# Performance work log

Measured on AMD Instinct MI355X. Metric: run time of the kernel, lower is better.

## Reference

```python
import jax, jax.numpy as jnp
import numpy as np
import math

B, S, D, H = 4, 2048, 1024, 16
DK = D // H  # 64
THETA = 10000.0


def setup_inputs() -> dict:
    key = jax.random.key(0)
    ks = jax.random.split(key, 5)
    std = 0.02
    return {
        "x": jax.random.normal(ks[0], (B, S, D), dtype=jnp.float32),
        "Wq": jax.random.normal(ks[1], (D, D), dtype=jnp.float32) * std,
        "Wk": jax.random.normal(ks[2], (D, D), dtype=jnp.float32) * std,
        "Wv": jax.random.normal(ks[3], (D, D), dtype=jnp.float32) * std,
        "Wo": jax.random.normal(ks[4], (D, D), dtype=jnp.float32) * std / math.sqrt(2 * 12),
        "token_positions": jnp.arange(S, dtype=jnp.int32),
    }


def _rope(x, pos):
    # x: [B, H, S, DK]; pos: [S]. Interleaved-pair rotary embedding.
    inv_freq = THETA ** (-jnp.arange(0, DK, 2, dtype=jnp.float32) / DK)  # [DK/2]
    ang = pos.astype(jnp.float32)[:, None] * inv_freq[None, :]  # [S, DK/2]
    cos, sin = jnp.cos(ang), jnp.sin(ang)
    x1, x2 = x[..., 0::2], x[..., 1::2]  # [B, H, S, DK/2]
    r1 = x1 * cos - x2 * sin
    r2 = x1 * sin + x2 * cos
    return jnp.stack([r1, r2], axis=-1).reshape(x.shape)


def reference(x, Wq, Wk, Wv, Wo, token_positions):
    b, s, d = x.shape
    Q = x @ Wq
    K = x @ Wk
    V = x @ Wv
    # [B, S, D] -> [B, H, S, DK]
    def split(t):
        return t.reshape(b, s, H, DK).transpose(0, 2, 1, 3)
    Qh, Kh, Vh = split(Q), split(K), split(V)
    Qh = _rope(Qh, token_positions)
    Kh = _rope(Kh, token_positions)
    scores = jnp.einsum('bhqd,bhkd->bhqk', Qh, Kh) / math.sqrt(DK)
    causal = jnp.tril(jnp.ones((s, s), dtype=bool))
    scores = jnp.where(causal, scores, -jnp.inf)
    probs = jax.nn.softmax(scores, axis=-1)
    out = jnp.einsum('bhqk,bhkd->bhqd', probs, Vh)
    out = out.transpose(0, 2, 1, 3).reshape(b, s, d)
    return out @ Wo
```

## Files before the change

kernel.cpp:

```cpp
#include <hip/hip_runtime.h>
#include <hip/hip_bf16.h>

#define B_N 4
#define S_LEN 2048
#define D_MODEL 1024
#define N_HEAD 16
#define D_HEAD 64
#define M_ROWS (B_N * S_LEN)

typedef short bf16x8 __attribute__((ext_vector_type(8)));
typedef short bf16x4 __attribute__((ext_vector_type(4)));
typedef float f32x4 __attribute__((ext_vector_type(4)));

#if __has_builtin(__builtin_amdgcn_mfma_f32_16x16x16bf16_1k)
#define HAVE_MFMA16 1
#else
#define HAVE_MFMA16 0
#endif

__device__ __forceinline__ unsigned short f2bf(float f) {
  union { float f; unsigned int u; } v; v.f = f;
  unsigned int r = v.u + 0x7FFFu + ((v.u >> 16) & 1u);
  return (unsigned short)(r >> 16);
}
__device__ __forceinline__ float bf2f(unsigned short u) {
  union { unsigned int u; float f; } v; v.u = ((unsigned int)u) << 16;
  return v.f;
}
__device__ __forceinline__ unsigned int pkbf(float a, float b) {
  union { __hip_bfloat162 h; unsigned int u; } cv;
  cv.h = __float22bfloat162_rn(make_float2(a, b));
  return cv.u;
}
__device__ __forceinline__ bf16x8 ld8(const unsigned short* p) {
  return *reinterpret_cast<const bf16x8*>(p);
}
__device__ __forceinline__ bf16x4 ld4(const unsigned short* p) {
  return *reinterpret_cast<const bf16x4*>(p);
}
__device__ __forceinline__ void glds16(const unsigned short* g, unsigned short* l) {
  __builtin_amdgcn_global_load_lds(
      (const __attribute__((address_space(1))) unsigned int*)g,
      (__attribute__((address_space(3))) unsigned int*)l, 16, 0, 0);
}

__global__ __launch_bounds__(256) void rope_tab_k(const int* __restrict__ pos,
                                                  float2* __restrict__ tab) {
  const int idx = blockIdx.x * 256 + threadIdx.x;
  const int s = idx >> 5;
  const int i = idx & 31;
  const float inv = exp2f(-(float)i * 0.41524101186092029f);
  const float ang = (float)pos[s] * inv;
  tab[idx] = make_float2(cosf(ang), sinf(ang));
}

__global__ __launch_bounds__(256) void cast_k(const float* __restrict__ X,
                                              unsigned short* __restrict__ Y) {
  const size_t i = ((size_t)blockIdx.x * 256 + threadIdx.x) * 8;
  const float4 a = *reinterpret_cast<const float4*>(X + i);
  const float4 b = *reinterpret_cast<const float4*>(X + i + 4);
  union { unsigned int u[4]; uint4 v; } o;
  o.u[0] = pkbf(a.x, a.y); o.u[1] = pkbf(a.z, a.w);
  o.u[2] = pkbf(b.x, b.y); o.u[3] = pkbf(b.z, b.w);
  *reinterpret_cast<uint4*>(Y + i) = o.v;
}

__global__ __launch_bounds__(256) void wtrans_k(
    const float* __restrict__ W0, const float* __restrict__ W1,
    const float* __restrict__ W2, const float* __restrict__ W3,
    unsigned short* __restrict__ T0, unsigned short* __restrict__ T1,
    unsigned short* __restrict__ T2, unsigned short* __restrict__ T3) {
  const int z = blockIdx.z;
  const float* __restrict__ W = (z == 0) ? W0 : (z == 1) ? W1 : (z == 2) ? W2 : W3;
  unsigned short* __restrict__ T = (z == 0) ? T0 : (z == 1) ? T1 : (z == 2) ? T2 : T3;
  __shared__ __align__(16) unsigned short tile[64][72];
  const int kb = blockIdx.x * 64;
  const int nb = blockIdx.y * 64;
#pragma unroll
  for (int it = 0; it < 2; ++it) {
    const int chunk = it * 256 + threadIdx.x;
    const int r = chunk >> 3;
    const int c8 = (chunk & 7) * 8;
    const float* src = W + (size_t)(kb + r) * D_MODEL + nb + c8;
    const float4 a = *reinterpret_cast<const float4*>(src);
    const float4 b = *reinterpret_cast<const float4*>(src + 4);
    union { unsigned int u[4]; uint4 v; } o;
    o.u[0] = pkbf(a.x, a.y); o.u[1] = pkbf(a.z, a.w);
    o.u[2] = pkbf(b.x, b.y); o.u[3] = pkbf(b.z, b.w);
    *reinterpret_cast<uint4*>(&tile[r][c8]) = o.v;
  }
  __syncthreads();
#pragma unroll
  for (int it = 0; it < 2; ++it) {
    const int chunk = it * 256 + threadIdx.x;
    const int n = chunk >> 3;
    const int k8 = (chunk & 7) * 8;
    __align__(16) unsigned short vals[8];
#pragma unroll
    for (int j = 0; j < 8; ++j) vals[j] = tile[k8 + j][n];
    *reinterpret_cast<uint4*>(T + (size_t)(nb + n) * D_MODEL + kb + k8) =
        *reinterpret_cast<const uint4*>(vals);
  }
}

__global__ __launch_bounds__(256) void gemm2_k(
    const unsigned short* __restrict__ A, const unsigned short* __restrict__ W,
    unsigned short* __restrict__ Qo, unsigned short* __restrict__ Ko,
    unsigned short* __restrict__ VTo, float* __restrict__ OF,
    const float2* __restrict__ tab, const int mode) {
  __shared__ __align__(16) unsigned short smem[4][64][68];
  unsigned short* As = &smem[0][0][0];
  unsigned short* Bs = As + 128 * 32;

  const int tid = threadIdx.x;
  const int lane = tid & 63;
  const int w = tid >> 6;
  const int l15 = lane & 15;
  const int l4 = lane >> 4;

  const int row0 = blockIdx.x * 128;
  const int col0 = blockIdx.y * 128;

  const int srow = w * 32 + (lane >> 2);
  const int scol = (lane & 3) * 8;
  const unsigned short* ga = A + (size_t)(row0 + srow) * D_MODEL + scol;
  const unsigned short* gb = W + (size_t)(col0 + srow) * D_MODEL + scol;
  unsigned short* la = &As[(w * 32) * 32];
  unsigned short* lb = &Bs[(w * 32) * 32];

  const int wrow = (w & 1) * 64;
  const int wcol = (w >> 1) * 64;

  f32x4 acc[4][4];
  const f32x4 fz = {0.f, 0.f, 0.f, 0.f};
#pragma unroll
  for (int m = 0; m < 4; ++m)
#pragma unroll
    for (int n = 0; n < 4; ++n) acc[m][n] = fz;

  for (int kb = 0; kb < D_MODEL; kb += 32) {
    glds16(ga + kb, la);
    glds16(ga + 16 * D_MODEL + kb, la + 16 * 32);
    glds16(gb + kb, lb);
    glds16(gb + 16 * D_MODEL + kb, lb + 16 * 32);
    __syncthreads();
    bf16x8 af[4], bfr[4];
#pragma unroll
    for (int m = 0; m < 4; ++m) af[m] = ld8(&As[(wrow + m * 16 + l15) * 32 + l4 * 8]);
#pragma unroll
    for (int n = 0; n < 4; ++n) bfr[n] = ld8(&Bs[(wcol + n * 16 + l15) * 32 + l4 * 8]);
#pragma unroll
    for (int m = 0; m < 4; ++m)
#pragma unroll
      for (int n = 0; n < 4; ++n)
        acc[m][n] = __builtin_amdgcn_mfma_f32_16x16x32_bf16(af[m], bfr[n], acc[m][n], 0, 0, 0);
    __syncthreads();
  }

  if (mode == 1) {
#pragma unroll
    for (int n = 0; n < 4; ++n) {
      const int gcol = col0 + wcol + n * 16 + l15;
#pragma unroll
      for (int m = 0; m < 4; ++m)
#pragma unroll
        for (int r = 0; r < 4; ++r)
          OF[(size_t)(row0 + wrow + m * 16 + l4 * 4 + r) * D_MODEL + gcol] = acc[m][n][r];
    }
    return;
  }
}

__global__ __launch_bounds__(512, 2) void gemm8_k(
    const unsigned short* __restrict__ A, const unsigned short* __restrict__ W,
    unsigned short* __restrict__ Qo, unsigned short* __restrict__ Ko,
    unsigned short* __restrict__ VTo, const float2* __restrict__ tab) {
  __shared__ __align__(16) unsigned short smem[2][2][256 * 64];

  const int tid = threadIdx.x;
  const int lane = tid & 63;
  const int w = tid >> 6;
  const int l15 = lane & 15;
  const int l4 = lane >> 4;
  const int wm = w >> 2;
  const int wn = w & 3;

  const int row0 = blockIdx.x * 256;
  const int col0 = blockIdx.y * 256;

  const int srow = lane >> 3;
  const int schunk = (lane & 7) ^ ((lane >> 4) & 2);
  const unsigned short* gA = A + (size_t)(row0 + w * 8 + srow) * D_MODEL + schunk * 8;
  const unsigned short* gB = W + (size_t)(col0 + w * 8 + srow) * D_MODEL + schunk * 8;

  const int kx = (l15 & 4) ? 16 : 0;
  const int kc0 = (l4 * 8) ^ kx;
  const int kc1 = (32 + l4 * 8) ^ kx;

  f32x4 acc[8][4];
  const f32x4 fz = {0.f, 0.f, 0.f, 0.f};
#pragma unroll
  for (int m = 0; m < 8; ++m)
#pragma unroll
    for (int n = 0; n < 4; ++n) acc[m][n] = fz;

#define G8_STAGE(SL, T)                                                        \
  do {                                                                         \
    asm volatile("" ::: "memory");                                             \
    const size_t ko_ = (size_t)(T) * 64;                                       \
    unsigned short* sa_ = &smem[SL][0][w * 512];                               \
    unsigned short* sb_ = &smem[SL][1][w * 512];                               \
    _Pragma("unroll") for (int j = 0; j < 4; ++j) {                            \
      glds16(gA + ko_ + (size_t)j * 64 * D_MODEL, sa_ + j * 4096);             \
      glds16(gB + ko_ + (size_t)j * 64 * D_MODEL, sb_ + j * 4096);             \
    }                                                                          \
    asm volatile("" ::: "memory");                                             \
  } while (0)

#define G8_PHASE(SL, MH, NH)                                                   \
  do {                                                                         \
    const unsigned short* As_ = &smem[SL][0][0];                               \
    const unsigned short* Bs_ = &smem[SL][1][0];                               \
    bf16x8 af_[4][2], bf_[2][2];                                               \
    _Pragma("unroll") for (int mi = 0; mi < 4; ++mi) {                         \
      const int rr_ = (wm * 128 + ((MH) * 4 + mi) * 16 + l15) * 64;            \
      af_[mi][0] = ld8(As_ + rr_ + kc0);                                       \
      af_[mi][1] = ld8(As_ + rr_ + kc1);                                       \
    }                                                                          \
    _Pragma("unroll") for (int ni = 0; ni < 2; ++ni) {                         \
      const int cc_ = (wn * 64 + ((NH) * 2 + ni) * 16 + l15) * 64;             \
      bf_[ni][0] = ld8(Bs_ + cc_ + kc0);                                       \
      bf_[ni][1] = ld8(Bs_ + cc_ + kc1);                                       \
    }                                                                          \
    __builtin_amdgcn_s_barrier();                                              \
    __builtin_amdgcn_s_setprio(1);                                             \
    _Pragma("unroll") for (int mi = 0; mi < 4; ++mi)                           \
      _Pragma("unroll") for (int ni = 0; ni < 2; ++ni) {                       \
        acc[(MH) * 4 + mi][(NH) * 2 + ni] =                                    \
            __builtin_amdgcn_mfma_f32_16x16x32_bf16(                           \
                af_[mi][0], bf_[ni][0], acc[(MH) * 4 + mi][(NH) * 2 + ni],     \
                0, 0, 0);                                                      \
        acc[(MH) * 4 + mi][(NH) * 2 + ni] =                                    \
            __builtin_amdgcn_mfma_f32_16x16x32_bf16(                           \
                af_[mi][1], bf_[ni][1], acc[(MH) * 4 + mi][(NH) * 2 + ni],     \
                0, 0, 0);                                                      \
      }                                                                        \
    __builtin_amdgcn_s_setprio(0);                                             \
    __builtin_amdgcn_s_barrier();                                              \
  } while (0)

  G8_STAGE(0, 0);
  G8_STAGE(1, 1);

  for (int i = 0; i < 8; ++i) {
    asm volatile("s_waitcnt vmcnt(8)" ::: "memory");
    __builtin_amdgcn_s_barrier();
    G8_PHASE(0, 0, 0);
    G8_PHASE(0, 0, 1);
    G8_PHASE(0, 1, 0);
    G8_PHASE(0, 1, 1);
    if (i < 7) {
      G8_STAGE(0, 2 * i + 2);
      asm volatile("s_waitcnt vmcnt(8)" ::: "memory");
    } else {
      asm volatile("s_waitcnt vmcnt(0)" ::: "memory");
    }
    __builtin_amdgcn_s_barrier();
    G8_PHASE(1, 0, 0);
    G8_PHASE(1, 0, 1);
    G8_PHASE(1, 1, 0);
    G8_PHASE(1, 1, 1);
    if (i < 7) G8_STAGE(1, 2 * i + 3);
  }
  asm volatile("" ::: "memory");

  unsigned short(*T)[68] =
      (unsigned short(*)[68])(&smem[0][0][0] + w * 4352);
  const int gcb = col0 + wn * 64;
  const bool isV = (gcb >= 2048);
  const int lr = lane >> 3;
  const int lc = lane & 7;

#pragma unroll
  for (int p = 0; p < 2; ++p) {
    if (!isV) {
#pragma unroll
      for (int mi = 0; mi < 4; ++mi)
#pragma unroll
        for (int n = 0; n < 4; ++n)
#pragma unroll
          for (int r = 0; r < 4; ++r)
            T[mi * 16 + l4 * 4 + r][n * 16 + l15] = f2bf(acc[p * 4 + mi][n][r]);
    } else {
#pragma unroll
      for (int mi = 0; mi < 4; ++mi)
#pragma unroll
        for (int n = 0; n < 4; ++n)
#pragma unroll
          for (int r = 0; r < 4; ++r)
            T[n * 16 + l15][mi * 16 + l4 * 4 + r] = f2bf(acc[p * 4 + mi][n][r]);
    }
    if (!isV) {
      const bool isQ = (gcb < 1024);
      unsigned short* O = isQ ? Qo : Ko;
      const float qs = isQ ? 0.18033688011112042f : 1.0f;
      const int cbase = gcb & 1023;
#pragma unroll
      for (int rg = 0; rg < 8; ++rg) {
        const int trow = rg * 8 + lr;
        const int grow = row0 + wm * 128 + p * 64 + trow;
        const int s = grow & (S_LEN - 1);
        const bf16x8 vv = ld8(&T[trow][lc * 8]);
        const float4 tA = *reinterpret_cast<const float4*>(&tab[s * 32 + lc * 4]);
        const float4 tB = *reinterpret_cast<const float4*>(&tab[s * 32 + lc * 4 + 2]);
        float x[8];
#pragma unroll
        for (int j = 0; j < 8; ++j) x[j] = bf2f((unsigned short)vv[j]);
        union { unsigned int u[4]; uint4 v; } o;
        o.u[0] = pkbf((x[0] * tA.x - x[1] * tA.y) * qs, (x[0] * tA.y + x[1] * tA.x) * qs);
        o.u[1] = pkbf((x[2] * tA.z - x[3] * tA.w) * qs, (x[2] * tA.w + x[3] * tA.z) * qs);
        o.u[2] = pkbf((x[4] * tB.x - x[5] * tB.y) * qs, (x[4] * tB.y + x[5] * tB.x) * qs);
        o.u[3] = pkbf((x[6] * tB.z - x[7] * tB.w) * qs, (x[6] * tB.w + x[7] * tB.z) * qs);
        *reinterpret_cast<uint4*>(O + (size_t)grow * D_MODEL + cbase + lc * 8) = o.v;
      }
    } else {
      const int vc0 = gcb - 2048;
      const int h = vc0 >> 6;
      const int bb = row0 >> 11;
      const int s0 = (row0 & (S_LEN - 1)) + wm * 128 + p * 64;
#pragma unroll
      for (int rg = 0; rg < 8; ++rg) {
        const int dk = rg * 8 + lr;
        const bf16x8 vv = ld8(&T[dk][lc * 8]);
        *reinterpret_cast<bf16x8*>(
            VTo + ((size_t)((bb << 4) + h) * 64 + dk) * S_LEN + s0 + lc * 8) = vv;
      }
    }
  }
#undef G8_STAGE
#undef G8_PHASE
}

__global__ __launch_bounds__(512) void attn6_k(
    const unsigned short* __restrict__ Q, const unsigned short* __restrict__ K,
    const unsigned short* __restrict__ VT, unsigned short* __restrict__ O) {
  const int pair = blockIdx.x;
  const int h = blockIdx.y;
  const int b = blockIdx.z;
  const int tid = threadIdx.x;
  const int w = tid >> 6;
  const int lane = tid & 63;
  const int l15 = lane & 15;
  const int l4 = lane >> 4;

  __shared__ __align__(16) unsigned short Ks[64][72];
  __shared__ __align__(16) unsigned short Vs[64][72];
#if !HAVE_MFMA16
  __shared__ __align__(16) unsigned short Ps[8][16][72];
#endif

  const f32x4 fz = {0.f, 0.f, 0.f, 0.f};
  const unsigned short* kbase = K + (size_t)b * S_LEN * D_MODEL + h * D_HEAD;
  const unsigned short* vbase = VT + (size_t)((b << 4) + h) * 64 * S_LEN;

  const int rr = tid >> 3;
  const int c8 = (tid & 7) * 8;

  for (int half = 0; half < 2; ++half) {
    const int qt = half ? (15 - pair) : pair;
    const int qb = qt * 128;
    const int qw0 = qb + w * 16;

    bf16x8 qf[2];
#pragma unroll
    for (int kc = 0; kc < 2; ++kc)
      qf[kc] = ld8(Q + (size_t)(b * S_LEN + qw0 + l15) * D_MODEL +
                   h * D_HEAD + kc * 32 + l4 * 8);

    f32x4 o[4];
#pragma unroll
    for (int d = 0; d < 4; ++d) o[d] = fz;
    float lsum = 0.f;

    const int nkt = qb / 64 + 2;
    uint4 kreg = *reinterpret_cast<const uint4*>(kbase + (size_t)rr * D_MODEL + c8);
    uint4 vreg = *reinterpret_cast<const uint4*>(vbase + (size_t)rr * S_LEN + c8);

    for (int kt = 0; kt < nkt; ++kt) {
      const int kb0 = kt * 64;
      *reinterpret_cast<uint4*>(&Ks[rr][c8]) = kreg;
      *reinterpret_cast<uint4*>(&Vs[rr][c8]) = vreg;
      if (kt + 1 < nkt) {
        const int nb0 = kb0 + 64;
        kreg = *reinterpret_cast<const uint4*>(kbase + (size_t)(nb0 + rr) * D_MODEL + c8);
        vreg = *reinterpret_cast<const uint4*>(vbase + (size_t)rr * S_LEN + nb0 + c8);
      }
      __syncthreads();

      if (kb0 <= qw0 + 15) {
        f32x4 s[4];
#pragma unroll
        for (int n = 0; n < 4; ++n) {
          const bf16x8 kf0 = ld8(&Ks[n * 16 + l15][l4 * 8]);
          const bf16x8 kf1 = ld8(&Ks[n * 16 + l15][32 + l4 * 8]);
          f32x4 a0 = __builtin_amdgcn_mfma_f32_16x16x32_bf16(kf0, qf[0], fz, 0, 0, 0);
          s[n] = __builtin_amdgcn_mfma_f32_16x16x32_bf16(kf1, qf[1], a0, 0, 0, 0);
        }
        bf16x4 pf[4];
        const bool full = (kb0 + 63 <= qw0);
        const int q = qw0 + l15;
        float su = lsum;
#pragma unroll
        for (int n = 0; n < 4; ++n) {
          float e[4];
          if (full) {
#pragma unroll
            for (int r = 0; r < 4; ++r) e[r] = exp2f(s[n][r]);
          } else {
#pragma unroll
            for (int r = 0; r < 4; ++r) {
              const int key = kb0 + n * 16 + l4 * 4 + r;
              const float v = exp2f(s[n][r]);
              e[r] = (key <= q) ? v : 0.f;
            }
          }
          su += (e[0] + e[1]) + (e[2] + e[3]);
          union { unsigned int u[2]; bf16x4 v; } pk;
          pk.u[0] = pkbf(e[0], e[1]);
          pk.u[1] = pkbf(e[2], e[3]);
          pf[n] = pk.v;
        }
        lsum = su;

#if HAVE_MFMA16
#pragma unroll
        for (int d = 0; d < 4; ++d) {
          bf16x4 vfc[4];
#pragma unroll
          for (int c = 0; c < 4; ++c) vfc[c] = ld4(&Vs[d * 16 + l15][c * 16 + l4 * 4]);
#pragma unroll
          for (int c = 0; c < 4; ++c)
            o[d] = __builtin_amdgcn_mfma_f32_16x16x16bf16_1k(vfc[c], pf[c], o[d], 0, 0, 0);
        }
#else
#pragma unroll
        for (int n = 0; n < 4; ++n)
          *reinterpret_cast<bf16x4*>(&Ps[w][l15][n * 16 + l4 * 4]) = pf[n];
        bf16x8 pfr[2];
#pragma unroll
        for (int kc = 0; kc < 2; ++kc)
          pfr[kc] = ld8(&Ps[w][l15][kc * 32 + l4 * 8]);
#pragma unroll
        for (int d = 0; d < 4; ++d) {
          const bf16x8 vf0 = ld8(&Vs[d * 16 + l15][l4 * 8]);
          const bf16x8 vf1 = ld8(&Vs[d * 16 + l15][32 + l4 * 8]);
          o[d] = __builtin_amdgcn_mfma_f32_16x16x32_bf16(vf0, pfr[0], o[d], 0, 0, 0);
          o[d] = __builtin_amdgcn_mfma_f32_16x16x32_bf16(vf1, pfr[1], o[d], 0, 0, 0);
        }
#endif
      }
      __syncthreads();
    }

    float s = lsum;
    s += __shfl_xor(s, 16);
    s += __shfl_xor(s, 32);
    const float li = 1.0f / s;
    unsigned short* op = O + (size_t)(b * S_LEN + qw0 + l15) * D_MODEL +
                         h * D_HEAD + l4 * 4;
#pragma unroll
    for (int d = 0; d < 4; ++d) {
      union { unsigned int u[2]; uint2 v; } ov;
      ov.u[0] = pkbf(o[d][0] * li, o[d][1] * li);
      ov.u[1] = pkbf(o[d][2] * li, o[d][3] * li);
      *reinterpret_cast<uint2*>(op + d * 16) = ov.v;
    }
  }
}

extern "C" void kernel_launch(void* const* d_in, const int* in_sizes, int n_in,
                              void* d_out, int out_size, void* d_ws, size_t ws_size,
                              hipStream_t stream) {
  const float* x  = (const float*)d_in[0];
  const float* Wq = (const float*)d_in[1];
  const float* Wk = (const float*)d_in[2];
  const float* Wv = (const float*)d_in[3];
  const float* Wo = (const float*)d_in[4];
  const int* pos  = (const int*)d_in[5];
  float* out = (float*)d_out;

  char* ws = (char*)d_ws;
  const size_t big = (size_t)M_ROWS * D_MODEL * 2;
  const size_t wsz = (size_t)D_MODEL * D_MODEL * 2;
  unsigned short* xb  = (unsigned short*)(ws + 0 * big);
  unsigned short* Qb  = (unsigned short*)(ws + 1 * big);
  unsigned short* Kb  = (unsigned short*)(ws + 2 * big);
  unsigned short* VT  = (unsigned short*)(ws + 3 * big);
  unsigned short* Wqkvt = (unsigned short*)(ws + 4 * big);
  unsigned short* Wot   = (unsigned short*)(ws + 4 * big + 3 * wsz);
  float2* tab = (float2*)d_out;

  rope_tab_k<<<dim3(S_LEN * 32 / 256), 256, 0, stream>>>(pos, tab);
  cast_k<<<dim3(M_ROWS * D_MODEL / 2048), 256, 0, stream>>>(x, xb);
  wtrans_k<<<dim3(16, 16, 4), 256, 0, stream>>>(
      Wq, Wk, Wv, Wo, Wqkvt, Wqkvt + (size_t)D_MODEL * D_MODEL,
      Wqkvt + 2 * (size_t)D_MODEL * D_MODEL, Wot);
  gemm8_k<<<dim3(M_ROWS / 256, 3 * D_MODEL / 256), 512, 0, stream>>>(
      xb, Wqkvt, Qb, Kb, VT, tab);
  attn6_k<<<dim3(8, N_HEAD, B_N), 512, 0, stream>>>(Qb, Kb, VT, Qb);
  gemm2_k<<<dim3(M_ROWS / 128, D_MODEL / 128), 256, 0, stream>>>(
      Qb, Wot, nullptr, nullptr, nullptr, out, nullptr, 1);
}
```

Baseline: 295.6 us.

## Interleave QKV GEMM global-to-LDS loads with MFMA phases at finer granularity

Rewrites the QKV projection GEMM pipeline. Each K-step's A/B tiles are split into half-tiles (128 rows), and one half-tile load is issued inside each compute phase, so loads are spread across all eight phases instead of issued in bulk between phase groups. The LDS swizzle is changed to an XOR over 8 chunks, and launch bounds drop to one block per CU. Also simplifies gemm2_k by removing unused mode parameters. The finer waitcnt scheduling is meant to hide global latency better, at the risk of more barriers and possible lower occupancy.

After: 456.0 us. 1.54x slower.

```diff
diff --git a/kernel.cpp b/kernel.cpp
--- a/kernel.cpp
+++ b/kernel.cpp
@@ -105,9 +105,7 @@
 
 __global__ __launch_bounds__(256) void gemm2_k(
     const unsigned short* __restrict__ A, const unsigned short* __restrict__ W,
-    unsigned short* __restrict__ Qo, unsigned short* __restrict__ Ko,
-    unsigned short* __restrict__ VTo, float* __restrict__ OF,
-    const float2* __restrict__ tab, const int mode) {
+    float* __restrict__ OF) {
   __shared__ __align__(16) unsigned short smem[4][64][68];
   unsigned short* As = &smem[0][0][0];
   unsigned short* Bs = As + 128 * 32;
@@ -157,25 +155,22 @@
     __syncthreads();
   }
 
-  if (mode == 1) {
-#pragma unroll
-    for (int n = 0; n < 4; ++n) {
-      const int gcol = col0 + wcol + n * 16 + l15;
-#pragma unroll
-      for (int m = 0; m < 4; ++m)
-#pragma unroll
-        for (int r = 0; r < 4; ++r)
-          OF[(size_t)(row0 + wrow + m * 16 + l4 * 4 + r) * D_MODEL + gcol] = acc[m][n][r];
-    }
-    return;
-  }
-}
-
-__global__ __launch_bounds__(512, 2) void gemm8_k(
+#pragma unroll
+  for (int n = 0; n < 4; ++n) {
+    const int gcol = col0 + wcol + n * 16 + l15;
+#pragma unroll
+    for (int m = 0; m < 4; ++m)
+#pragma unroll
+      for (int r = 0; r < 4; ++r)
+        OF[(size_t)(row0 + wrow + m * 16 + l4 * 4 + r) * D_MODEL + gcol] = acc[m][n][r];
+  }
+}
+
+__global__ __launch_bounds__(512, 1) void gemm9_k(
     const unsigned short* __restrict__ A, const unsigned short* __restrict__ W,
     unsigned short* __restrict__ Qo, unsigned short* __restrict__ Ko,
     unsigned short* __restrict__ VTo, const float2* __restrict__ tab) {
-  __shared__ __align__(16) unsigned short smem[2][2][256 * 64];
+  __shared__ __align__(16) unsigned short smem[2][2][2][128 * 64];
 
   const int tid = threadIdx.x;
   const int lane = tid & 63;
@@ -184,18 +179,20 @@
   const int l4 = lane >> 4;
   const int wm = w >> 2;
   const int wn = w & 3;
+  const int hb = wn >> 1;
+  const int rbb = (wn & 1) * 64;
 
   const int row0 = blockIdx.x * 256;
   const int col0 = blockIdx.y * 256;
 
-  const int srow = lane >> 3;
-  const int schunk = (lane & 7) ^ ((lane >> 4) & 2);
-  const unsigned short* gA = A + (size_t)(row0 + w * 8 + srow) * D_MODEL + schunk * 8;
-  const unsigned short* gB = W + (size_t)(col0 + w * 8 + srow) * D_MODEL + schunk * 8;
-
-  const int kx = (l15 & 4) ? 16 : 0;
-  const int kc0 = (l4 * 8) ^ kx;
-  const int kc1 = (32 + l4 * 8) ^ kx;
+  const int srow8 = lane >> 3;
+  const int schunk = (lane & 7) ^ srow8;
+  const unsigned short* gA = A + (size_t)(row0 + w * 16 + srow8) * D_MODEL + schunk * 8;
+  const unsigned short* gB = W + (size_t)(col0 + w * 16 + srow8) * D_MODEL + schunk * 8;
+
+  const int swz = l15 & 7;
+  const int kc0 = (l4 ^ swz) * 8;
+  const int kc1 = ((l4 + 4) ^ swz) * 8;
 
   f32x4 acc[8][4];
   const f32x4 fz = {0.f, 0.f, 0.f, 0.f};
@@ -204,78 +201,87 @@
 #pragma unroll
     for (int n = 0; n < 4; ++n) acc[m][n] = fz;
 
-#define G8_STAGE(SL, T)                                                        \
+#define STG(SL, AB, HA, T)                                                     \
   do {                                                                         \
-    asm volatile("" ::: "memory");                                             \
-    const size_t ko_ = (size_t)(T) * 64;                                       \
-    unsigned short* sa_ = &smem[SL][0][w * 512];                               \
-    unsigned short* sb_ = &smem[SL][1][w * 512];                               \
-    _Pragma("unroll") for (int j = 0; j < 4; ++j) {                            \
-      glds16(gA + ko_ + (size_t)j * 64 * D_MODEL, sa_ + j * 4096);             \
-      glds16(gB + ko_ + (size_t)j * 64 * D_MODEL, sb_ + j * 4096);             \
-    }                                                                          \
-    asm volatile("" ::: "memory");                                             \
+    const unsigned short* g_ =                                                 \
+        ((AB) ? gB : gA) + (size_t)(HA) * 128 * D_MODEL + (size_t)(T) * 64;    \
+    unsigned short* d_ = &smem[SL][AB][HA][w * 1024];                          \
+    glds16(g_, d_);                                                            \
+    glds16(g_ + 8 * D_MODEL, d_ + 512);                                        \
   } while (0)
 
-#define G8_PHASE(SL, MH, NH)                                                   \
+#define PH(SL, QM, QN, STGX, TAILW)                                            \
   do {                                                                         \
-    const unsigned short* As_ = &smem[SL][0][0];                               \
-    const unsigned short* Bs_ = &smem[SL][1][0];                               \
     bf16x8 af_[4][2], bf_[2][2];                                               \
     _Pragma("unroll") for (int mi = 0; mi < 4; ++mi) {                         \
-      const int rr_ = (wm * 128 + ((MH) * 4 + mi) * 16 + l15) * 64;            \
-      af_[mi][0] = ld8(As_ + rr_ + kc0);                                       \
-      af_[mi][1] = ld8(As_ + rr_ + kc1);                                       \
+      const int ra_ = ((QM) * 64 + mi * 16 + l15) * 64;                        \
+      af_[mi][0] = ld8(&smem[SL][0][wm][ra_ + kc0]);                           \
+      af_[mi][1] = ld8(&smem[SL][0][wm][ra_ + kc1]);                           \
     }                                                                          \
     _Pragma("unroll") for (int ni = 0; ni < 2; ++ni) {                         \
-      const int cc_ = (wn * 64 + ((NH) * 2 + ni) * 16 + l15) * 64;             \
-      bf_[ni][0] = ld8(Bs_ + cc_ + kc0);                                       \
-      bf_[ni][1] = ld8(Bs_ + cc_ + kc1);                                       \
+      const int rb_ = (rbb + (QN) * 32 + ni * 16 + l15) * 64;                  \
+      bf_[ni][0] = ld8(&smem[SL][1][hb][rb_ + kc0]);                           \
+      bf_[ni][1] = ld8(&smem[SL][1][hb][rb_ + kc1]);                           \
     }                                                                          \
+    STGX;                                                                      \
     __builtin_amdgcn_s_barrier();                                              \
     __builtin_amdgcn_s_setprio(1);                                             \
     _Pragma("unroll") for (int mi = 0; mi < 4; ++mi)                           \
       _Pragma("unroll") for (int ni = 0; ni < 2; ++ni) {                       \
-        acc[(MH) * 4 + mi][(NH) * 2 + ni] =                                    \
+        acc[(QM) * 4 + mi][(QN) * 2 + ni] =                                    \
             __builtin_amdgcn_mfma_f32_16x16x32_bf16(                           \
-                af_[mi][0], bf_[ni][0], acc[(MH) * 4 + mi][(NH) * 2 + ni],     \
+                af_[mi][0], bf_[ni][0], acc[(QM) * 4 + mi][(QN) * 2 + ni],     \
                 0, 0, 0);                                                      \
-        acc[(MH) * 4 + mi][(NH) * 2 + ni] =                                    \
+        acc[(QM) * 4 + mi][(QN) * 2 + ni] =                                    \
             __builtin_amdgcn_mfma_f32_16x16x32_bf16(                           \
-                af_[mi][1], bf_[ni][1], acc[(MH) * 4 + mi][(NH) * 2 + ni],     \
+                af_[mi][1], bf_[ni][1], acc[(QM) * 4 + mi][(QN) * 2 + ni],     \
                 0, 0, 0);                                                      \
       }                                                                        \
     __builtin_amdgcn_s_setprio(0);                                             \
+    TAILW;                                                                     \
     __builtin_amdgcn_s_barrier();                                              \
   } while (0)
 
-  G8_STAGE(0, 0);
-  G8_STAGE(1, 1);
+#define VM2 asm volatile("s_waitcnt vmcnt(2)" ::: "memory")
+#define VM0 asm volatile("s_waitcnt vmcnt(0)" ::: "memory")
+#define NOP ((void)0)
+
+  STG(0, 0, 0, 0); STG(0, 1, 0, 0); STG(0, 0, 1, 0); STG(0, 1, 1, 0);
+  STG(1, 0, 0, 1);
+  VM2;
+  __builtin_amdgcn_s_barrier();
 
   for (int i = 0; i < 8; ++i) {
-    asm volatile("s_waitcnt vmcnt(8)" ::: "memory");
-    __builtin_amdgcn_s_barrier();
-    G8_PHASE(0, 0, 0);
-    G8_PHASE(0, 0, 1);
-    G8_PHASE(0, 1, 0);
-    G8_PHASE(0, 1, 1);
+    const int v = 2 * i + 1;
+    const int u2 = 2 * i + 2;
     if (i < 7) {
-      G8_STAGE(0, 2 * i + 2);
-      asm volatile("s_waitcnt vmcnt(8)" ::: "memory");
+      PH(0, 0, 0, STG(1, 1, 0, v), NOP);
+      PH(0, 0, 1, STG(1, 0, 1, v), NOP);
+      PH(0, 1, 0, STG(1, 1, 1, v), NOP);
+      PH(0, 1, 1, STG(0, 0, 0, u2), VM2);
+      PH(1, 0, 0, STG(0, 1, 0, u2), NOP);
+      PH(1, 0, 1, STG(0, 0, 1, u2), NOP);
+      PH(1, 1, 0, STG(0, 1, 1, u2), NOP);
+      PH(1, 1, 1, STG(1, 0, 0, u2 + 1), VM2);
     } else {
-      asm volatile("s_waitcnt vmcnt(0)" ::: "memory");
+      PH(0, 0, 0, STG(1, 1, 0, v), NOP);
+      PH(0, 0, 1, STG(1, 0, 1, v), NOP);
+      PH(0, 1, 0, STG(1, 1, 1, v), NOP);
+      PH(0, 1, 1, NOP, VM0);
+      PH(1, 0, 0, NOP, NOP);
+      PH(1, 0, 1, NOP, NOP);
+      PH(1, 1, 0, NOP, NOP);
+      PH(1, 1, 1, NOP, NOP);
     }
-    __builtin_amdgcn_s_barrier();
-    G8_PHASE(1, 0, 0);
-    G8_PHASE(1, 0, 1);
-    G8_PHASE(1, 1, 0);
-    G8_PHASE(1, 1, 1);
-    if (i < 7) G8_STAGE(1, 2 * i + 3);
-  }
-  asm volatile("" ::: "memory");
+  }
+#undef STG
+#undef PH
+#undef VM2
+#undef VM0
+#undef NOP
 
   unsigned short(*T)[68] =
-      (unsigned short(*)[68])(&smem[0][0][0] + w * 4352);
+      (unsigned short(*)[68])((unsigned short*)smem + w * 4352);
   const int gcb = col0 + wn * 64;
   const bool isV = (gcb >= 2048);
   const int lr = lane >> 3;
@@ -337,8 +343,6 @@
       }
     }
   }
-#undef G8_STAGE
-#undef G8_PHASE
 }
 
 __global__ __launch_bounds__(512) void attn6_k(
@@ -505,9 +509,8 @@
   wtrans_k<<<dim3(16, 16, 4), 256, 0, stream>>>(
       Wq, Wk, Wv, Wo, Wqkvt, Wqkvt + (size_t)D_MODEL * D_MODEL,
       Wqkvt + 2 * (size_t)D_MODEL * D_MODEL, Wot);
-  gemm8_k<<<dim3(M_ROWS / 256, 3 * D_MODEL / 256), 512, 0, stream>>>(
+  gemm9_k<<<dim3(M_ROWS / 256, 3 * D_MODEL / 256), 512, 0, stream>>>(
       xb, Wqkvt, Qb, Kb, VT, tab);
   attn6_k<<<dim3(8, N_HEAD, B_N), 512, 0, stream>>>(Qb, Kb, VT, Qb);
-  gemm2_k<<<dim3(M_ROWS / 128, D_MODEL / 128), 256, 0, stream>>>(
-      Qb, Wot, nullptr, nullptr, nullptr, out, nullptr, 1);
-}
+  gemm2_k<<<dim3(M_ROWS / 128, D_MODEL / 128), 256, 0, stream>>>(Qb, Wot, out);
+}
```
